# Kernel optimization log

Hardware: AMD Instinct MI355X
Metric: run time of the kernel (lower is better)

## Reference

```python
import jax, jax.numpy as jnp
import numpy as np

S = 20  # number of standard amino acids; hardcoded in the original layer


def expm_fixed(A, squarings=6, terms=14):
    """Scaling-and-squaring matrix exponential with fixed squaring count.
    A: (..., n, n). tau*Q entries are small (tau ~ softplus(-3)), so a fixed
    2^-6 scaling + Taylor-14 matches tf.linalg.expm to fp32 tolerance."""
    A = A / (2.0 ** squarings)
    I = jnp.broadcast_to(jnp.eye(A.shape[-1], dtype=A.dtype), A.shape)
    out = I
    term = I
    for i in range(1, terms + 1):
        term = jnp.matmul(term, A) / i
        out = out + term
    for _ in range(squarings):
        out = jnp.matmul(out, out)
    return out


def make_rate_matrix(R, p, eps=1e-16):
    """R: (N, s, s) symmetric exchangeabilities, zero diag. p: (N, s) equilibrium."""
    Q = R * p[:, None, :]                       # Q[i,j] = R[i,j] * p[j]
    diag = jnp.sum(Q, axis=-1, keepdims=True)   # (N, s, 1)
    eye = jnp.eye(Q.shape[-1], dtype=Q.dtype)
    Q = Q - diag * eye
    mue = jnp.sum(p[:, :, None] * diag, axis=-2, keepdims=True)  # (N,1,1)
    return Q / jnp.maximum(mue, eps)


def setup_inputs() -> dict:
    key = jax.random.key(0)
    ks = jax.random.split(key, 6)
    m, b, L, k, nr = 2, 256, 1024, 4, 100
    inputs = jax.random.uniform(ks[0], (m, b, L, S), dtype=jnp.float32)
    rate_indices = jax.random.randint(ks[1], (m, b), 0, nr, dtype=jnp.int64)
    # rate_init = constant(-3.0); small jitter so gradients are non-degenerate
    tau_kernel = -3.0 + 0.1 * jax.random.normal(ks[2], (m, nr), dtype=jnp.float32)
    exchangeability_kernel = 0.1 * jax.random.normal(ks[3], (m, k, S, S), dtype=jnp.float32)
    equilibrium_kernel = 0.1 * jax.random.normal(ks[4], (m, k, S), dtype=jnp.float32)
    per_matrix_rates_kernel = 0.1 * jax.random.normal(ks[5], (m, k), dtype=jnp.float32)
    return {
        "inputs": inputs,
        "tau_kernel": tau_kernel,
        "exchangeability_kernel": exchangeability_kernel,
        "equilibrium_kernel": equilibrium_kernel,
        "per_matrix_rates_kernel": per_matrix_rates_kernel,
        "rate_indices": rate_indices,
    }


def reference(inputs, tau_kernel, exchangeability_kernel, equilibrium_kernel,
              per_matrix_rates_kernel, rate_indices):
    m, b, L, s = inputs.shape
    k = exchangeability_kernel.shape[1]
    # make_tau(subset): gather per-sequence times then softplus
    tau = jax.nn.softplus(jnp.take_along_axis(tau_kernel, rate_indices, axis=1))  # (m,b)
    # per-matrix rates
    pmr = jax.nn.softplus(per_matrix_rates_kernel)  # (m,k)
    mut_rates = tau[:, :, None] * pmr[:, None, :]   # (m,b,k)
    # make_R: symmetrize, softplus, zero diagonal
    K = exchangeability_kernel
    R = jax.nn.softplus(0.5 * (K + jnp.swapaxes(K, -1, -2)))
    R = R * (1.0 - jnp.eye(s, dtype=R.dtype))       # (m,k,s,s)
    # make_p
    p = jax.nn.softmax(equilibrium_kernel, axis=-1)  # (m,k,s)
    # normalized rate matrices
    Q = make_rate_matrix(R.reshape(-1, s, s), p.reshape(-1, s)).reshape(m, k, s, s)
    # tau * Q, batched over sequences: (m,b,k,s,s)
    tauQ = mut_rates[..., None, None] * Q[:, None]
    P = expm_fixed(tauQ.reshape(-1, s, s)).reshape(m, b, k, s, s)
    # vector-format inputs path (non-transposed): mbLz,mbkzs->mbLks
    anc = jnp.einsum('mblz,mbkzs->mblks', inputs, P)
    # documented output: (num_model, b, L, num_matrices*s)
    return anc.reshape(m, b, L, k * s)
```

## Files before the change

kernel.cpp:

```cpp
#include <hip/hip_runtime.h>
#include <math.h>

#define M_  2
#define B_  256
#define L_  1024
#define K_  4
#define S_  20
#define NR_ 100
#define NTERM 7

typedef float f32x4_t __attribute__((ext_vector_type(4)));

__device__ __forceinline__ float softplusf(float x) {
    return x > 20.0f ? x : log1pf(expf(x));
}

__global__ __launch_bounds__(512)
void qpow_kernel(const float* __restrict__ exch,
                 const float* __restrict__ equil,
                 float*       __restrict__ Qpow)
{
    __shared__ float sQ[400];
    __shared__ float sT[2][400];
    __shared__ float sRow[20];

    const int blk = blockIdx.x;
    const int kk = blk % K_;
    const int mm = blk / K_;
    const int tid = threadIdx.x;
    const bool act = tid < 400;
    const int i = tid / 20;
    const int j = tid - i * 20;

    float p[20];
    float Q0 = 0.0f, rowsum = 0.0f;

    if (act) {
        const float* eq = equil + (mm * K_ + kk) * S_;
        float mx = eq[0];
        #pragma unroll
        for (int z = 1; z < 20; ++z) mx = fmaxf(mx, eq[z]);
        float s = 0.0f;
        #pragma unroll
        for (int z = 0; z < 20; ++z) { p[z] = expf(eq[z] - mx); s += p[z]; }
        const float inv = 1.0f / s;
        #pragma unroll
        for (int z = 0; z < 20; ++z) p[z] *= inv;

        const float* Kx = exch + (mm * K_ + kk) * S_ * S_;
        float R = (i == j) ? 0.0f : softplusf(0.5f * (Kx[i * 20 + j] + Kx[j * 20 + i]));
        Q0 = R * p[j];
        sQ[tid] = Q0;
    }
    __syncthreads();

    if (act) {
        rowsum = 0.0f;
        #pragma unroll
        for (int z = 0; z < 20; ++z) rowsum += sQ[i * 20 + z];
        if (j == 0) sRow[i] = rowsum;
    }
    __syncthreads();

    float* Tout = Qpow + (size_t)blk * (NTERM * 400);
    if (act) {
        float mue = 0.0f;
        #pragma unroll
        for (int z = 0; z < 20; ++z) mue += p[z] * sRow[z];
        float q = (Q0 - ((i == j) ? rowsum : 0.0f)) / fmaxf(mue, 1e-16f);
        sQ[tid] = q;
        sT[0][tid] = q;
        Tout[tid] = q;
    }
    __syncthreads();

    int cur = 0;
    for (int n = 2; n <= NTERM; ++n) {
        if (act) {
            float acc = 0.0f;
            #pragma unroll
            for (int z = 0; z < 20; ++z) acc += sT[cur][i * 20 + z] * sQ[z * 20 + j];
            acc /= (float)n;
            sT[cur ^ 1][tid] = acc;
            Tout[(n - 1) * 400 + tid] = acc;
        }
        __syncthreads();
        cur ^= 1;
    }
}

__global__ __launch_bounds__(512)
void pbuild_kernel(const float* __restrict__ Qpow,
                   const float* __restrict__ tauk,
                   const float* __restrict__ pmrk,
                   float*       __restrict__ Pws)
{
    const int blk = blockIdx.x;
    const int kk = blk % K_;
    const int rr = (blk / K_) % NR_;
    const int mm = blk / (K_ * NR_);
    const int tid = threadIdx.x;
    if (tid >= 400) return;

    const float mu = softplusf(tauk[mm * NR_ + rr]) * softplusf(pmrk[mm * K_ + kk]);
    const float* T = Qpow + ((size_t)(mm * K_ + kk) * NTERM) * 400 + tid;

    float acc = (tid % 21 == 0) ? 1.0f : 0.0f;
    float mp = mu;
    #pragma unroll
    for (int n = 0; n < NTERM; ++n) { acc = fmaf(mp, T[n * 400], acc); mp *= mu; }
    Pws[(size_t)blk * 400 + tid] = acc;
}

#define SPANR 256
#define TPB3  320

__device__ __forceinline__ void fma4(float4& a, float s, const float4& p) {
    a.x = fmaf(s, p.x, a.x);
    a.y = fmaf(s, p.y, a.y);
    a.z = fmaf(s, p.z, a.z);
    a.w = fmaf(s, p.w, a.w);
}

__device__ __forceinline__ void nt_store4(float* dst, const float4& v) {
    f32x4_t w;
    w.x = v.x; w.y = v.y; w.z = v.z; w.w = v.w;
    __builtin_nontemporal_store(w, (f32x4_t*)dst);
}

__global__ __launch_bounds__(TPB3)
void einsum_kernel(const float* __restrict__ inp,
                   const float* __restrict__ Pws,
                   const int*   __restrict__ ridx,
                   float*       __restrict__ out)
{
    const int bx      = blockIdx.x;
    const int quarter = bx & 3;
    const int mb      = bx >> 2;
    const int mm      = mb >> 8;
    const int tid     = threadIdx.x;
    const int t       = tid % 20;
    const int rg      = tid / 20;
    const int k       = t / 5;
    const int s0      = (t % 5) * 4;

    const int r = ridx[mb];

    const float* Pbase = Pws + ((size_t)(mm * NR_ + r) * K_ + k) * 400 + s0;
    float4 Pf[20];
    #pragma unroll
    for (int z = 0; z < 20; ++z)
        Pf[z] = *(const float4*)(Pbase + z * 20);

    const size_t row0 = (size_t)mb * L_ + (size_t)quarter * SPANR;
    const float* inb = inp + row0 * 20;
    float*       ob  = out + row0 * 80 + k * 20 + s0;

    #pragma unroll 1
    for (int c = 0; c < 8; ++c) {
        const int l0 = rg + (c * 2 + 0) * 16;
        const int l1 = rg + (c * 2 + 1) * 16;
        float4 a0 = make_float4(0.f, 0.f, 0.f, 0.f);
        float4 a1 = make_float4(0.f, 0.f, 0.f, 0.f);

        #pragma unroll
        for (int z4 = 0; z4 < 5; ++z4) {
            const float4 v0 = *(const float4*)(inb + l0 * 20 + z4 * 4);
            const float4 v1 = *(const float4*)(inb + l1 * 20 + z4 * 4);
            fma4(a0, v0.x, Pf[z4 * 4 + 0]);
            fma4(a0, v0.y, Pf[z4 * 4 + 1]);
            fma4(a0, v0.z, Pf[z4 * 4 + 2]);
            fma4(a0, v0.w, Pf[z4 * 4 + 3]);
            fma4(a1, v1.x, Pf[z4 * 4 + 0]);
            fma4(a1, v1.y, Pf[z4 * 4 + 1]);
            fma4(a1, v1.z, Pf[z4 * 4 + 2]);
            fma4(a1, v1.w, Pf[z4 * 4 + 3]);
        }

        nt_store4(ob + (size_t)l0 * 80, a0);
        nt_store4(ob + (size_t)l1 * 80, a1);
    }
}

extern "C" void kernel_launch(void* const* d_in, const int* in_sizes, int n_in,
                              void* d_out, int out_size, void* d_ws, size_t ws_size,
                              hipStream_t stream) {
    const float* inp   = (const float*)d_in[0];
    const float* tauk  = (const float*)d_in[1];
    const float* exch  = (const float*)d_in[2];
    const float* equil = (const float*)d_in[3];
    const float* pmrk  = (const float*)d_in[4];
    const int*   ridx  = (const int*)d_in[5];
    float* outp = (float*)d_out;

    float* Qpow = (float*)d_ws;
    float* Pws  = Qpow + (size_t)M_ * K_ * NTERM * 400;

    qpow_kernel<<<M_ * K_, 512, 0, stream>>>(exch, equil, Qpow);
    pbuild_kernel<<<M_ * NR_ * K_, 512, 0, stream>>>(Qpow, tauk, pmrk, Pws);
    einsum_kernel<<<M_ * B_ * (L_ / SPANR), TPB3, 0, stream>>>(inp, Pws, ridx, outp);
}
```

Measured before the change: 63.17 us.

## Fuse P construction into einsum kernel and restructure row loop

Removes the separate pbuild kernel launch and builds each block's 20x80 P tile in shared memory from the precomputed Q powers. Every einsum block now recomputes the Taylor polynomial for its sequence, which adds redundant work (2048 blocks times 1600 entries times 7 terms) in exchange for one fewer launch and no global round trip for P. The inner loop now reads P from LDS per z-slice and processes 8 rows per chunk instead of keeping P in 80 registers, which lowers register pressure but adds LDS reads.

```diff
diff --git a/kernel.cpp b/kernel.cpp
--- a/kernel.cpp
+++ b/kernel.cpp
@@ -89,29 +89,6 @@
     }
 }
 
-__global__ __launch_bounds__(512)
-void pbuild_kernel(const float* __restrict__ Qpow,
-                   const float* __restrict__ tauk,
-                   const float* __restrict__ pmrk,
-                   float*       __restrict__ Pws)
-{
-    const int blk = blockIdx.x;
-    const int kk = blk % K_;
-    const int rr = (blk / K_) % NR_;
-    const int mm = blk / (K_ * NR_);
-    const int tid = threadIdx.x;
-    if (tid >= 400) return;
-
-    const float mu = softplusf(tauk[mm * NR_ + rr]) * softplusf(pmrk[mm * K_ + kk]);
-    const float* T = Qpow + ((size_t)(mm * K_ + kk) * NTERM) * 400 + tid;
-
-    float acc = (tid % 21 == 0) ? 1.0f : 0.0f;
-    float mp = mu;
-    #pragma unroll
-    for (int n = 0; n < NTERM; ++n) { acc = fmaf(mp, T[n * 400], acc); mp *= mu; }
-    Pws[(size_t)blk * 400 + tid] = acc;
-}
-
 #define SPANR 256
 #define TPB3  320
 
@@ -130,10 +107,14 @@
 
 __global__ __launch_bounds__(TPB3)
 void einsum_kernel(const float* __restrict__ inp,
-                   const float* __restrict__ Pws,
+                   const float* __restrict__ Qpow,
+                   const float* __restrict__ tauk,
+                   const float* __restrict__ pmrk,
                    const int*   __restrict__ ridx,
                    float*       __restrict__ out)
 {
+    __shared__ float Pl[20 * 80];
+
     const int bx      = blockIdx.x;
     const int quarter = bx & 3;
     const int mb      = bx >> 2;
@@ -146,39 +127,59 @@
 
     const int r = ridx[mb];
 
-    const float* Pbase = Pws + ((size_t)(mm * NR_ + r) * K_ + k) * 400 + s0;
-    float4 Pf[20];
-    #pragma unroll
-    for (int z = 0; z < 20; ++z)
-        Pf[z] = *(const float4*)(Pbase + z * 20);
+    {
+        const float tau = softplusf(tauk[mm * NR_ + r]);
+        #pragma unroll
+        for (int q = 0; q < 5; ++q) {
+            const int idx = tid + q * TPB3;
+            const int z   = idx / 80;
+            const int rem = idx - z * 80;
+            const int kk  = rem / 20;
+            const int j   = rem - kk * 20;
+            const float mu = tau * softplusf(pmrk[mm * K_ + kk]);
+            const float* T = Qpow + ((size_t)(mm * K_ + kk) * NTERM) * 400 + z * 20 + j;
+            float acc = (z == j) ? 1.0f : 0.0f;
+            float mp = mu;
+            #pragma unroll
+            for (int n = 0; n < NTERM; ++n) { acc = fmaf(mp, T[n * 400], acc); mp *= mu; }
+            Pl[idx] = acc;
+        }
+    }
+    __syncthreads();
 
     const size_t row0 = (size_t)mb * L_ + (size_t)quarter * SPANR;
     const float* inb = inp + row0 * 20;
     float*       ob  = out + row0 * 80 + k * 20 + s0;
+    const float* Pt  = Pl + k * 20 + s0;
 
     #pragma unroll 1
-    for (int c = 0; c < 8; ++c) {
-        const int l0 = rg + (c * 2 + 0) * 16;
-        const int l1 = rg + (c * 2 + 1) * 16;
-        float4 a0 = make_float4(0.f, 0.f, 0.f, 0.f);
-        float4 a1 = make_float4(0.f, 0.f, 0.f, 0.f);
+    for (int cc = 0; cc < 2; ++cc) {
+        float4 acc[8];
+        #pragma unroll
+        for (int r8 = 0; r8 < 8; ++r8) acc[r8] = make_float4(0.f, 0.f, 0.f, 0.f);
 
         #pragma unroll
         for (int z4 = 0; z4 < 5; ++z4) {
-            const float4 v0 = *(const float4*)(inb + l0 * 20 + z4 * 4);
-            const float4 v1 = *(const float4*)(inb + l1 * 20 + z4 * 4);
-            fma4(a0, v0.x, Pf[z4 * 4 + 0]);
-            fma4(a0, v0.y, Pf[z4 * 4 + 1]);
-            fma4(a0, v0.z, Pf[z4 * 4 + 2]);
-            fma4(a0, v0.w, Pf[z4 * 4 + 3]);
-            fma4(a1, v1.x, Pf[z4 * 4 + 0]);
-            fma4(a1, v1.y, Pf[z4 * 4 + 1]);
-            fma4(a1, v1.z, Pf[z4 * 4 + 2]);
-            fma4(a1, v1.w, Pf[z4 * 4 + 3]);
-        }
-
-        nt_store4(ob + (size_t)l0 * 80, a0);
-        nt_store4(ob + (size_t)l1 * 80, a1);
+            const float4 p0 = *(const float4*)(Pt + (z4 * 4 + 0) * 80);
+            const float4 p1 = *(const float4*)(Pt + (z4 * 4 + 1) * 80);
+            const float4 p2 = *(const float4*)(Pt + (z4 * 4 + 2) * 80);
+            const float4 p3 = *(const float4*)(Pt + (z4 * 4 + 3) * 80);
+            #pragma unroll
+            for (int r8 = 0; r8 < 8; ++r8) {
+                const int l = rg + (cc * 8 + r8) * 16;
+                const float4 av = *(const float4*)(inb + l * 20 + z4 * 4);
+                fma4(acc[r8], av.x, p0);
+                fma4(acc[r8], av.y, p1);
+                fma4(acc[r8], av.z, p2);
+                fma4(acc[r8], av.w, p3);
+            }
+        }
+
+        #pragma unroll
+        for (int r8 = 0; r8 < 8; ++r8) {
+            const int l = rg + (cc * 8 + r8) * 16;
+            nt_store4(ob + (size_t)l * 80, acc[r8]);
+        }
     }
 }
 
@@ -194,9 +195,7 @@
     float* outp = (float*)d_out;
 
     float* Qpow = (float*)d_ws;
-    float* Pws  = Qpow + (size_t)M_ * K_ * NTERM * 400;
 
     qpow_kernel<<<M_ * K_, 512, 0, stream>>>(exch, equil, Qpow);
-    pbuild_kernel<<<M_ * NR_ * K_, 512, 0, stream>>>(Qpow, tauk, pmrk, Pws);
-    einsum_kernel<<<M_ * B_ * (L_ / SPANR), TPB3, 0, stream>>>(inp, Pws, ridx, outp);
-}
+    einsum_kernel<<<M_ * B_ * (L_ / SPANR), TPB3, 0, stream>>>(inp, Qpow, tauk, pmrk, ridx, outp);
+}
```

Result: slower. 115.9 us (+83.4%).

## Stage P and input tile in shared memory, accumulate all rows before storing

Applied to the files above, without the earlier changes.

The einsum kernel now cooperatively copies the four 20x20 P matrices and the block's 256x20 input tile into shared memory with coalesced float4 loads. Each thread then keeps 16 row accumulators in registers and reads P and inputs from LDS, instead of holding P in registers and doing redundant strided global loads per row. All stores are issued at the end. This trades register pressure and about 36KB of LDS per block for fewer, coalesced global reads, but may reduce occupancy and remove load/compute overlap within the block.

```diff
diff --git a/kernel.cpp b/kernel.cpp
--- a/kernel.cpp
+++ b/kernel.cpp
@@ -134,6 +134,9 @@
                    const int*   __restrict__ ridx,
                    float*       __restrict__ out)
 {
+    __shared__ float Pl[K_ * 400];
+    __shared__ float inL[SPANR * 20];
+
     const int bx      = blockIdx.x;
     const int quarter = bx & 3;
     const int mb      = bx >> 2;
@@ -146,39 +149,49 @@
 
     const int r = ridx[mb];
 
-    const float* Pbase = Pws + ((size_t)(mm * NR_ + r) * K_ + k) * 400 + s0;
-    float4 Pf[20];
-    #pragma unroll
-    for (int z = 0; z < 20; ++z)
-        Pf[z] = *(const float4*)(Pbase + z * 20);
+    {
+        const float4* Psrc = (const float4*)(Pws + ((size_t)(mm * NR_ + r) * K_) * 400);
+        float4* Pd = (float4*)Pl;
+        Pd[tid] = Psrc[tid];
+        if (tid < 80) Pd[320 + tid] = Psrc[320 + tid];
+
+        const size_t row0g = (size_t)mb * L_ + (size_t)quarter * SPANR;
+        const float4* Isrc = (const float4*)(inp + row0g * 20);
+        float4* Id = (float4*)inL;
+        #pragma unroll
+        for (int q = 0; q < 4; ++q) Id[tid + q * TPB3] = Isrc[tid + q * TPB3];
+    }
+    __syncthreads();
 
     const size_t row0 = (size_t)mb * L_ + (size_t)quarter * SPANR;
-    const float* inb = inp + row0 * 20;
-    float*       ob  = out + row0 * 80 + k * 20 + s0;
-
-    #pragma unroll 1
-    for (int c = 0; c < 8; ++c) {
-        const int l0 = rg + (c * 2 + 0) * 16;
-        const int l1 = rg + (c * 2 + 1) * 16;
-        float4 a0 = make_float4(0.f, 0.f, 0.f, 0.f);
-        float4 a1 = make_float4(0.f, 0.f, 0.f, 0.f);
-
-        #pragma unroll
-        for (int z4 = 0; z4 < 5; ++z4) {
-            const float4 v0 = *(const float4*)(inb + l0 * 20 + z4 * 4);
-            const float4 v1 = *(const float4*)(inb + l1 * 20 + z4 * 4);
-            fma4(a0, v0.x, Pf[z4 * 4 + 0]);
-            fma4(a0, v0.y, Pf[z4 * 4 + 1]);
-            fma4(a0, v0.z, Pf[z4 * 4 + 2]);
-            fma4(a0, v0.w, Pf[z4 * 4 + 3]);
-            fma4(a1, v1.x, Pf[z4 * 4 + 0]);
-            fma4(a1, v1.y, Pf[z4 * 4 + 1]);
-            fma4(a1, v1.z, Pf[z4 * 4 + 2]);
-            fma4(a1, v1.w, Pf[z4 * 4 + 3]);
+    float* ob = out + row0 * 80 + k * 20 + s0;
+    const float* Pk = Pl + k * 400 + s0;
+
+    float4 acc[16];
+    #pragma unroll
+    for (int rr = 0; rr < 16; ++rr) acc[rr] = make_float4(0.f, 0.f, 0.f, 0.f);
+
+    #pragma unroll
+    for (int z4 = 0; z4 < 5; ++z4) {
+        const float4 p0 = *(const float4*)(Pk + (z4 * 4 + 0) * 20);
+        const float4 p1 = *(const float4*)(Pk + (z4 * 4 + 1) * 20);
+        const float4 p2 = *(const float4*)(Pk + (z4 * 4 + 2) * 20);
+        const float4 p3 = *(const float4*)(Pk + (z4 * 4 + 3) * 20);
+        #pragma unroll
+        for (int rr = 0; rr < 16; ++rr) {
+            const int l = rg + rr * 16;
+            const float4 av = *(const float4*)(inL + l * 20 + z4 * 4);
+            fma4(acc[rr], av.x, p0);
+            fma4(acc[rr], av.y, p1);
+            fma4(acc[rr], av.z, p2);
+            fma4(acc[rr], av.w, p3);
         }
-
-        nt_store4(ob + (size_t)l0 * 80, a0);
-        nt_store4(ob + (size_t)l1 * 80, a1);
+    }
+
+    #pragma unroll
+    for (int rr = 0; rr < 16; ++rr) {
+        const int l = rg + rr * 16;
+        nt_store4(ob + (size_t)l * 80, acc[rr]);
     }
 }
 
```

Result: faster. 57.69 us (-8.7%).
